# Optimization experiments

Hardware: AMD Instinct MI355X
Metric: run time of the kernel (lower is better)

## Reference

```python
import jax, jax.numpy as jnp
import numpy as np

B = 65536
IN_F = 1024
OUT_F = 1024
N_ACT = 4  # len(activation_functions): tanh, sin, relu, sigmoid (cyclic over columns)


def setup_inputs() -> dict:
    key = jax.random.key(0)
    k1, k2 = jax.random.split(key)
    x = jax.random.normal(k1, (B, IN_F), dtype=jnp.float32)
    # xavier_uniform for weight [out, in]
    limit = float(np.sqrt(6.0 / (IN_F + OUT_F)))
    W = jax.random.uniform(k2, (OUT_F, IN_F), dtype=jnp.float32, minval=-limit, maxval=limit)
    b = jnp.zeros((OUT_F,), dtype=jnp.float32)
    return {"input": x, "W": W, "b": b}


def _apply_cyclic_acts(y):
    # column i gets activation (i % N_ACT); OUT_F % N_ACT == 0 so reshape to groups
    Bb, O = y.shape
    yg = y.reshape(Bb, O // N_ACT, N_ACT)
    out = jnp.stack([
        jnp.tanh(yg[..., 0]),
        jnp.sin(yg[..., 1]),
        jax.nn.relu(yg[..., 2]),
        jax.nn.sigmoid(yg[..., 3]),
    ], axis=-1)
    return out.reshape(Bb, O)


def reference(input, W, b) -> jnp.ndarray:
    y = jnp.einsum('bi,oi->bo', input, W) + b  # F.linear
    return _apply_cyclic_acts(y)
```

## Files before the change

kernel.cpp:

```cpp
#include <hip/hip_runtime.h>

constexpr int B_ROWS = 65536;
constexpr int IN_F   = 1024;
constexpr int OUT_F  = 1024;

constexpr int BDIM = 512;
constexpr int BM = 256, BN = 256, BK = 64;

typedef __bf16 bf16x8 __attribute__((ext_vector_type(8)));
typedef float  f32x4  __attribute__((ext_vector_type(4)));

__device__ __forceinline__ bf16x8 cvt8(f32x4 u0, f32x4 u1) {
    bf16x8 v;
    v[0] = (__bf16)u0[0]; v[1] = (__bf16)u0[1]; v[2] = (__bf16)u0[2]; v[3] = (__bf16)u0[3];
    v[4] = (__bf16)u1[0]; v[5] = (__bf16)u1[1]; v[6] = (__bf16)u1[2]; v[7] = (__bf16)u1[3];
    return v;
}

__device__ __forceinline__ void glds16(const __bf16* g, unsigned char* l) {
    __builtin_amdgcn_global_load_lds(
        (const __attribute__((address_space(1))) unsigned int*)(const void*)g,
        (__attribute__((address_space(3))) unsigned int*)(void*)l,
        16, 0, 0);
}

__global__ __launch_bounds__(256)
void w_to_bf16(const float* __restrict__ W, __bf16* __restrict__ Wb) {
    const size_t i = ((size_t)blockIdx.x * 256 + threadIdx.x) * 16;
    f32x4 a0 = *(const f32x4*)(W + i);
    f32x4 a1 = *(const f32x4*)(W + i + 4);
    f32x4 a2 = *(const f32x4*)(W + i + 8);
    f32x4 a3 = *(const f32x4*)(W + i + 12);
    *(bf16x8*)(Wb + i)     = cvt8(a0, a1);
    *(bf16x8*)(Wb + i + 8) = cvt8(a2, a3);
}


__global__ __launch_bounds__(BDIM, 2)
void fused_linear_act(const float* __restrict__ X,
                      const __bf16* __restrict__ Wb,
                      const float* __restrict__ bias,
                      float* __restrict__ O)
{
    __shared__ __attribute__((aligned(16))) unsigned char lds[2 * 65536];

    const int bx  = blockIdx.x;
    const int xcd = bx & 7;
    const int idx = bx >> 3;
    const int nt  = idx & 3;
    const int mt  = xcd + 8 * (idx >> 2);
    const int m0 = mt * BM;
    const int n0 = nt * BN;

    const int tid  = threadIdx.x;
    const int lane = tid & 63;
    const int wave = tid >> 6;
    const int wm2  = (wave >> 2) * 128;
    const int wn2  = (wave & 3) * 64;
    const int lrow = lane & 15;
    const int quad = lane >> 4;

    const int arow = tid >> 1;
    const int ah   = tid & 1;
    const float* asrc = X + (size_t)(m0 + arow) * IN_F + ah * 32;
    const int awr = ah * 16384 + (arow >> 4) * 1024 + (arow & 15) * 16;

    const __bf16* bs0 = Wb + (size_t)(n0 + (wave & 3) * 64 + lrow) * IN_F
                           + (wave >> 2) * 32 + quad * 8;
    const __bf16* bs1 = bs0 + (size_t)16 * IN_F;
    const __bf16* bs2 = bs0 + (size_t)32 * IN_F;
    const __bf16* bs3 = bs0 + (size_t)48 * IN_F;
    const int bdst = 32768 + (wave >> 2) * 16384 + (wave & 3) * 4096;

    const int rdA = (wave >> 2) * 8192 + lane * 16;
    const int rdB = 32768 + (wave & 3) * 4096 + lane * 16;

    unsigned char* const b0 = lds;
    unsigned char* const b1 = lds + 65536;

    f32x4 acc[8][4];
    #pragma unroll
    for (int i = 0; i < 8; ++i)
        #pragma unroll
        for (int j = 0; j < 4; ++j)
            acc[i][j] = (f32x4){0.f, 0.f, 0.f, 0.f};

    f32x4 ar0, ar1, ar2, ar3, ar4, ar5, ar6, ar7;
    bf16x8 aq0, aq1, aq2, aq3, bq0, bq1, bq2, bq3;

#define ALOAD_LO(KA) do { \
    ar0 = *(const f32x4*)(asrc + (KA));      ar1 = *(const f32x4*)(asrc + (KA) + 4);  \
    ar2 = *(const f32x4*)(asrc + (KA) + 8);  ar3 = *(const f32x4*)(asrc + (KA) + 12); } while (0)
#define ALOAD_HI(KA) do { \
    ar4 = *(const f32x4*)(asrc + (KA) + 16); ar5 = *(const f32x4*)(asrc + (KA) + 20); \
    ar6 = *(const f32x4*)(asrc + (KA) + 24); ar7 = *(const f32x4*)(asrc + (KA) + 28); } while (0)
#define DSW(NXTB) do { unsigned char* _w = (NXTB) + awr; \
    *(bf16x8*)(_w)       = cvt8(ar0, ar1); \
    *(bf16x8*)(_w + 256) = cvt8(ar2, ar3); \
    *(bf16x8*)(_w + 512) = cvt8(ar4, ar5); \
    *(bf16x8*)(_w + 768) = cvt8(ar6, ar7); } while (0)
#define GLDSB(NXTB, KB) do { unsigned char* _d = (NXTB) + bdst; \
    glds16(bs0 + (KB), _d);        glds16(bs1 + (KB), _d + 1024); \
    glds16(bs2 + (KB), _d + 2048); glds16(bs3 + (KB), _d + 3072); } while (0)
#define READ_A(CURB, KS, MH) do { \
    const unsigned char* _ra = (CURB) + rdA + (KS) * 16384 + (MH) * 4096; \
    aq0 = *(const bf16x8*)(_ra);        aq1 = *(const bf16x8*)(_ra + 1024); \
    aq2 = *(const bf16x8*)(_ra + 2048); aq3 = *(const bf16x8*)(_ra + 3072); } while (0)
#define READ_B(CURB, KS) do { \
    const unsigned char* _rb = (CURB) + rdB + (KS) * 16384; \
    bq0 = *(const bf16x8*)(_rb);        bq1 = *(const bf16x8*)(_rb + 1024); \
    bq2 = *(const bf16x8*)(_rb + 2048); bq3 = *(const bf16x8*)(_rb + 3072); } while (0)
#define MFMA1(MH, I, J) acc[(MH)*4+(I)][(J)] = \
    __builtin_amdgcn_mfma_f32_16x16x32_bf16(aq##I, bq##J, acc[(MH)*4+(I)][(J)], 0, 0, 0)
#define MFMAQ(MH) do { __builtin_amdgcn_s_setprio(1); \
    MFMA1(MH,0,0); MFMA1(MH,0,1); MFMA1(MH,0,2); MFMA1(MH,0,3); \
    MFMA1(MH,1,0); MFMA1(MH,1,1); MFMA1(MH,1,2); MFMA1(MH,1,3); \
    MFMA1(MH,2,0); MFMA1(MH,2,1); MFMA1(MH,2,2); MFMA1(MH,2,3); \
    MFMA1(MH,3,0); MFMA1(MH,3,1); MFMA1(MH,3,2); MFMA1(MH,3,3); \
    __builtin_amdgcn_s_setprio(0); } while (0)
#define VM8    asm volatile("s_waitcnt vmcnt(8)" ::: "memory")
#define VM0    asm volatile("s_waitcnt vmcnt(0)" ::: "memory")
#define VMNONE ((void)0)

#define ROUND(CURB, NXTB, DO_GLDS, KB, DO_DSW, DO_ALOAD, KA, VMW) do { \
     \
    if (DO_GLDS) GLDSB(NXTB, KB); \
    READ_B(CURB, 0); READ_A(CURB, 0, 0); \
    __builtin_amdgcn_s_barrier(); \
    MFMAQ(0); \
     \
    if (DO_DSW) DSW(NXTB); \
    if (DO_ALOAD) ALOAD_LO(KA); \
    READ_A(CURB, 0, 1); \
    __builtin_amdgcn_s_barrier(); \
    MFMAQ(1); \
     \
    if (DO_ALOAD) ALOAD_HI(KA); \
    READ_B(CURB, 1); READ_A(CURB, 1, 0); \
    __builtin_amdgcn_s_barrier(); \
    MFMAQ(0); \
     \
    READ_A(CURB, 1, 1); \
    asm volatile("s_waitcnt lgkmcnt(0)" ::: "memory"); \
    VMW; \
    __builtin_amdgcn_s_barrier(); \
    MFMAQ(1); \
} while (0)

    ALOAD_LO(0); ALOAD_HI(0);
    GLDSB(b0, 0);
    DSW(b0);
    ALOAD_LO(64); ALOAD_HI(64);
    asm volatile("s_waitcnt vmcnt(8) lgkmcnt(0)" ::: "memory");
    __builtin_amdgcn_s_barrier();

    #pragma unroll 1
    for (int t = 0; t < 14; t += 2) {
        const int kb0 = (t + 1) * 64, ka0 = (t + 2) * 64;
        ROUND(b0, b1, true, kb0, true, true, ka0, VM8);
        const int kb1 = (t + 2) * 64, ka1 = (t + 3) * 64;
        ROUND(b1, b0, true, kb1, true, true, ka1, VM8);
    }
    ROUND(b0, b1, true, 15 * 64, true, false, 0, VM0);
    ROUND(b1, b0, false, 0, false, false, 0, VMNONE);

    const int s = lane & 3;
    const float kmul = (s == 0) ? -2.f : -1.f;
    const float aa   = (s == 0) ?  2.f :  1.f;
    const float cc   = (s == 0) ? -1.f :  0.f;
    const bool  is_sin  = (s == 1);
    const bool  is_relu = (s == 2);

    float bv[4];
    #pragma unroll
    for (int fn = 0; fn < 4; ++fn) bv[fn] = bias[n0 + wn2 + fn * 16 + lrow];

    #pragma unroll
    for (int fm = 0; fm < 8; ++fm) {
        #pragma unroll
        for (int r = 0; r < 4; ++r) {
            const int gr = m0 + wm2 + fm * 16 + quad * 4 + r;
            float* op = O + (size_t)gr * OUT_F + n0 + wn2 + lrow;
            #pragma unroll
            for (int fn = 0; fn < 4; ++fn) {
                const float y = acc[fm][fn][r] + bv[fn];
                const float e = __expf(kmul * y);
                const float g = fmaf(aa, __builtin_amdgcn_rcpf(1.f + e), cc);
                const float sv = __sinf(y);
                const float rv = fmaxf(y, 0.f);
                const float res = is_sin ? sv : (is_relu ? rv : g);
                op[fn * 16] = res;
            }
        }
    }
}

extern "C" void kernel_launch(void* const* d_in, const int* in_sizes, int n_in,
                              void* d_out, int out_size, void* d_ws, size_t ws_size,
                              hipStream_t stream) {
    const float* X = (const float*)d_in[0];
    const float* W = (const float*)d_in[1];
    const float* b = (const float*)d_in[2];
    float* O = (float*)d_out;
    __bf16* Wb = (__bf16*)d_ws;

    const size_t nW = (size_t)OUT_F * IN_F;
    w_to_bf16<<<(int)(nW / (256 * 16)), 256, 0, stream>>>(W, Wb);

    const int grid = (B_ROWS / BM) * (OUT_F / BN);
    fused_linear_act<<<grid, BDIM, 0, stream>>>(X, Wb, b, O);
}
```

Baseline: 598.0 us.

## Restructure GEMM main loop with front-loaded staging and double barriers per MFMA phase

Each round now issues all B global-to-LDS loads and A LDS writes for the opposite buffer at its start, instead of spreading them across phases. The B tile load mapping changes so each wave loads 32 rows covering both K halves. Each MFMA quarter is wrapped in a barrier before and after, so waves march in lockstep. The aim is cleaner overlap between memory and MFMA, at the cost of twice as many barriers per round.

```diff
diff --git a/kernel.cpp b/kernel.cpp
--- a/kernel.cpp
+++ b/kernel.cpp
@@ -35,7 +35,6 @@
     *(bf16x8*)(Wb + i + 8) = cvt8(a2, a3);
 }
 
-
 __global__ __launch_bounds__(BDIM, 2)
 void fused_linear_act(const float* __restrict__ X,
                       const __bf16* __restrict__ Wb,
@@ -55,8 +54,8 @@
     const int tid  = threadIdx.x;
     const int lane = tid & 63;
     const int wave = tid >> 6;
-    const int wm2  = (wave >> 2) * 128;
-    const int wn2  = (wave & 3) * 64;
+    const int wr2  = wave >> 2;
+    const int w4   = wave & 3;
     const int lrow = lane & 15;
     const int quad = lane >> 4;
 
@@ -65,15 +64,7 @@
     const float* asrc = X + (size_t)(m0 + arow) * IN_F + ah * 32;
     const int awr = ah * 16384 + (arow >> 4) * 1024 + (arow & 15) * 16;
 
-    const __bf16* bs0 = Wb + (size_t)(n0 + (wave & 3) * 64 + lrow) * IN_F
-                           + (wave >> 2) * 32 + quad * 8;
-    const __bf16* bs1 = bs0 + (size_t)16 * IN_F;
-    const __bf16* bs2 = bs0 + (size_t)32 * IN_F;
-    const __bf16* bs3 = bs0 + (size_t)48 * IN_F;
-    const int bdst = 32768 + (wave >> 2) * 16384 + (wave & 3) * 4096;
-
-    const int rdA = (wave >> 2) * 8192 + lane * 16;
-    const int rdB = 32768 + (wave & 3) * 4096 + lane * 16;
+    const __bf16* bgp = Wb + (size_t)(n0 + 32 * wave + lrow) * IN_F + quad * 8;
 
     unsigned char* const b0 = lds;
     unsigned char* const b1 = lds + 65536;
@@ -94,22 +85,23 @@
 #define ALOAD_HI(KA) do { \
     ar4 = *(const f32x4*)(asrc + (KA) + 16); ar5 = *(const f32x4*)(asrc + (KA) + 20); \
     ar6 = *(const f32x4*)(asrc + (KA) + 24); ar7 = *(const f32x4*)(asrc + (KA) + 28); } while (0)
-#define DSW(NXTB) do { unsigned char* _w = (NXTB) + awr; \
+#define DSW(BUF) do { unsigned char* _w = (BUF) + awr; \
     *(bf16x8*)(_w)       = cvt8(ar0, ar1); \
     *(bf16x8*)(_w + 256) = cvt8(ar2, ar3); \
     *(bf16x8*)(_w + 512) = cvt8(ar4, ar5); \
     *(bf16x8*)(_w + 768) = cvt8(ar6, ar7); } while (0)
-#define GLDSB(NXTB, KB) do { unsigned char* _d = (NXTB) + bdst; \
-    glds16(bs0 + (KB), _d);        glds16(bs1 + (KB), _d + 1024); \
-    glds16(bs2 + (KB), _d + 2048); glds16(bs3 + (KB), _d + 3072); } while (0)
-#define READ_A(CURB, KS, MH) do { \
-    const unsigned char* _ra = (CURB) + rdA + (KS) * 16384 + (MH) * 4096; \
-    aq0 = *(const bf16x8*)(_ra);        aq1 = *(const bf16x8*)(_ra + 1024); \
-    aq2 = *(const bf16x8*)(_ra + 2048); aq3 = *(const bf16x8*)(_ra + 3072); } while (0)
-#define READ_B(CURB, KS) do { \
-    const unsigned char* _rb = (CURB) + rdB + (KS) * 16384; \
-    bq0 = *(const bf16x8*)(_rb);        bq1 = *(const bf16x8*)(_rb + 1024); \
-    bq2 = *(const bf16x8*)(_rb + 2048); bq3 = *(const bf16x8*)(_rb + 3072); } while (0)
+#define GBALL(BUF, K) do { unsigned char* _d0 = (BUF) + 32768 + wave * 2048; \
+    unsigned char* _d1 = _d0 + 16384; \
+    glds16(bgp + (K), _d0);      glds16(bgp + (K) + 16 * IN_F, _d0 + 1024); \
+    glds16(bgp + (K) + 32, _d1); glds16(bgp + (K) + 32 + 16 * IN_F, _d1 + 1024); } while (0)
+#define RA(BUF, KH, MH) do { \
+    const unsigned char* _r = (BUF) + (KH) * 16384 + (wr2 * 8 + (MH) * 4) * 1024 + lane * 16; \
+    aq0 = *(const bf16x8*)(_r);        aq1 = *(const bf16x8*)(_r + 1024); \
+    aq2 = *(const bf16x8*)(_r + 2048); aq3 = *(const bf16x8*)(_r + 3072); } while (0)
+#define RB(BUF, KH) do { \
+    const unsigned char* _r = (BUF) + 32768 + (KH) * 16384 + (w4 * 4) * 1024 + lane * 16; \
+    bq0 = *(const bf16x8*)(_r);        bq1 = *(const bf16x8*)(_r + 1024); \
+    bq2 = *(const bf16x8*)(_r + 2048); bq3 = *(const bf16x8*)(_r + 3072); } while (0)
 #define MFMA1(MH, I, J) acc[(MH)*4+(I)][(J)] = \
     __builtin_amdgcn_mfma_f32_16x16x32_bf16(aq##I, bq##J, acc[(MH)*4+(I)][(J)], 0, 0, 0)
 #define MFMAQ(MH) do { __builtin_amdgcn_s_setprio(1); \
@@ -118,51 +110,35 @@
     MFMA1(MH,2,0); MFMA1(MH,2,1); MFMA1(MH,2,2); MFMA1(MH,2,3); \
     MFMA1(MH,3,0); MFMA1(MH,3,1); MFMA1(MH,3,2); MFMA1(MH,3,3); \
     __builtin_amdgcn_s_setprio(0); } while (0)
-#define VM8    asm volatile("s_waitcnt vmcnt(8)" ::: "memory")
-#define VM0    asm volatile("s_waitcnt vmcnt(0)" ::: "memory")
-#define VMNONE ((void)0)
+#define BAR() __builtin_amdgcn_s_barrier()
+#define VM8() asm volatile("s_waitcnt vmcnt(8)" ::: "memory")
+#define VM0() asm volatile("s_waitcnt vmcnt(0)" ::: "memory")
+#define VMNONE() ((void)0)
 
-#define ROUND(CURB, NXTB, DO_GLDS, KB, DO_DSW, DO_ALOAD, KA, VMW) do { \
-     \
-    if (DO_GLDS) GLDSB(NXTB, KB); \
-    READ_B(CURB, 0); READ_A(CURB, 0, 0); \
-    __builtin_amdgcn_s_barrier(); \
-    MFMAQ(0); \
-     \
-    if (DO_DSW) DSW(NXTB); \
-    if (DO_ALOAD) ALOAD_LO(KA); \
-    READ_A(CURB, 0, 1); \
-    __builtin_amdgcn_s_barrier(); \
-    MFMAQ(1); \
-     \
-    if (DO_ALOAD) ALOAD_HI(KA); \
-    READ_B(CURB, 1); READ_A(CURB, 1, 0); \
-    __builtin_amdgcn_s_barrier(); \
-    MFMAQ(0); \
-     \
-    READ_A(CURB, 1, 1); \
-    asm volatile("s_waitcnt lgkmcnt(0)" ::: "memory"); \
-    VMW; \
-    __builtin_amdgcn_s_barrier(); \
-    MFMAQ(1); \
+#define ROUND(CUR, OPP, DO_STAGE, KB1, DO_ALOAD, KA2, VMW) do { \
+     if (DO_STAGE) { GBALL(OPP, KB1); DSW(OPP); } \
+             RB(CUR, 0); RA(CUR, 0, 0); BAR(); MFMAQ(0); BAR(); \
+     if (DO_ALOAD) ALOAD_LO(KA2); \
+             RA(CUR, 0, 1); BAR(); MFMAQ(1); BAR(); \
+     if (DO_ALOAD) ALOAD_HI(KA2); \
+             RB(CUR, 1); RA(CUR, 1, 0); BAR(); MFMAQ(0); BAR(); \
+     RA(CUR, 1, 1); BAR(); MFMAQ(1); VMW(); BAR(); \
 } while (0)
 
     ALOAD_LO(0); ALOAD_HI(0);
-    GLDSB(b0, 0);
+    GBALL(b0, 0);
     DSW(b0);
     ALOAD_LO(64); ALOAD_HI(64);
     asm volatile("s_waitcnt vmcnt(8) lgkmcnt(0)" ::: "memory");
-    __builtin_amdgcn_s_barrier();
+    BAR();
 
     #pragma unroll 1
     for (int t = 0; t < 14; t += 2) {
-        const int kb0 = (t + 1) * 64, ka0 = (t + 2) * 64;
-        ROUND(b0, b1, true, kb0, true, true, ka0, VM8);
-        const int kb1 = (t + 2) * 64, ka1 = (t + 3) * 64;
-        ROUND(b1, b0, true, kb1, true, true, ka1, VM8);
+        ROUND(b0, b1, true, (t + 1) * 64, true, (t + 2) * 64, VM8);
+        ROUND(b1, b0, true, (t + 2) * 64, true, (t + 3) * 64, VM8);
     }
-    ROUND(b0, b1, true, 15 * 64, true, false, 0, VM0);
-    ROUND(b1, b0, false, 0, false, false, 0, VMNONE);
+    ROUND(b0, b1, true, 15 * 64, false, 0, VM0);
+    ROUND(b1, b0, false, 0, false, 0, VMNONE);
 
     const int s = lane & 3;
     const float kmul = (s == 0) ? -2.f : -1.f;
@@ -173,14 +149,14 @@
 
     float bv[4];
     #pragma unroll
-    for (int fn = 0; fn < 4; ++fn) bv[fn] = bias[n0 + wn2 + fn * 16 + lrow];
+    for (int fn = 0; fn < 4; ++fn) bv[fn] = bias[n0 + w4 * 64 + fn * 16 + lrow];
 
     #pragma unroll
     for (int fm = 0; fm < 8; ++fm) {
         #pragma unroll
         for (int r = 0; r < 4; ++r) {
-            const int gr = m0 + wm2 + fm * 16 + quad * 4 + r;
-            float* op = O + (size_t)gr * OUT_F + n0 + wn2 + lrow;
+            const int gr = m0 + wr2 * 128 + fm * 16 + quad * 4 + r;
+            float* op = O + (size_t)gr * OUT_F + n0 + w4 * 64 + lrow;
             #pragma unroll
             for (int fn = 0; fn < 4; ++fn) {
                 const float y = acc[fm][fn][r] + bv[fn];
```

Result: slower. 613.8 us (+2.6%).
